# Optimization experiments

Hardware: AMD Instinct MI355X
Metric: run time of the kernel (lower is better)

## Reference

```python
import jax, jax.numpy as jnp
import numpy as np

EPS = 1e-5
NUM_HEADS = 16
HEAD_DIM = 64


def layernorm(x, g, b):
    mu = jnp.mean(x, axis=-1, keepdims=True)
    var = jnp.mean(jnp.square(x - mu), axis=-1, keepdims=True)
    return (x - mu) * jax.lax.rsqrt(var + EPS) * g + b


def setup_inputs() -> dict:
    key = jax.random.key(0)
    ks = jax.random.split(key, 10)
    B, S, Q, D = 4, 4096, 256, 1024
    x = jax.random.normal(ks[0], (B, S, D), dtype=jnp.float32)
    queries = jax.random.normal(ks[1], (B, Q, D), dtype=jnp.float32)
    attn_mask = jax.random.randint(ks[2], (B, NUM_HEADS, Q, S), 0, 2) == 1
    key_padding_mask = jax.random.randint(ks[3], (B, S), 0, 2) == 1
    scale = 1.0 / np.sqrt(2.0 * D)  # xavier-ish
    Wq = jax.random.normal(ks[4], (D, D), dtype=jnp.float32) * scale
    Wk = jax.random.normal(ks[5], (D, D), dtype=jnp.float32) * scale
    Wv = jax.random.normal(ks[6], (D, D), dtype=jnp.float32) * scale
    Wo = jax.random.normal(ks[7], (D, D), dtype=jnp.float32) * scale
    ln1_g = jnp.ones((D,), jnp.float32); ln1_b = jnp.zeros((D,), jnp.float32)
    ln2_g = jnp.ones((D,), jnp.float32); ln2_b = jnp.zeros((D,), jnp.float32)
    return {"x": x, "queries": queries, "attn_mask": attn_mask,
            "key_padding_mask": key_padding_mask, "Wq": Wq, "Wk": Wk,
            "Wv": Wv, "Wo": Wo, "ln1_g": ln1_g, "ln1_b": ln1_b,
            "ln2_g": ln2_g, "ln2_b": ln2_b}


def reference(x, queries, attn_mask, key_padding_mask, Wq, Wk, Wv, Wo,
              ln1_g, ln1_b, ln2_g, ln2_b):
    B, S, D = x.shape
    Q = queries.shape[1]
    H, hd = NUM_HEADS, HEAD_DIM

    xn = layernorm(x, ln1_g, ln1_b)
    q = (queries @ Wq.T).reshape(B, Q, H, hd)
    k = (xn @ Wk.T).reshape(B, S, H, hd)
    v = (xn @ Wv.T).reshape(B, S, H, hd)

    # scores: (B, H, Q, S)
    scores = jnp.einsum('bqhd,bshd->bhqs', q, k) / np.sqrt(hd)

    mask = attn_mask | key_padding_mask[:, None, None, :]
    neg_inf = jnp.float32(-jnp.inf)
    masked = jnp.where(mask, neg_inf, scores)
    all_masked = jnp.all(mask, axis=-1, keepdims=True)  # rows fully masked
    safe = jnp.where(all_masked, 0.0, masked)
    attn = jax.nn.softmax(safe, axis=-1)
    attn = jnp.where(all_masked, 0.0, attn)

    out = jnp.einsum('bhqs,bshd->bqhd', attn, v).reshape(B, Q, D)
    out = layernorm(out, ln2_g, ln2_b)
    return out @ Wo.T, attn.mean(axis=1)
```

## Files before the change

kernel.cpp:

```cpp
#include <hip/hip_runtime.h>
#include <math.h>

#define DEV __device__ __forceinline__

typedef float  f4v  __attribute__((ext_vector_type(4)));
typedef __bf16 b8v  __attribute__((ext_vector_type(8)));
typedef short  s8v  __attribute__((ext_vector_type(8)));

DEV short f2b(float f){ __bf16 h = (__bf16)f; return __builtin_bit_cast(short, h); }
DEV float b2f(short s){ __bf16 h = __builtin_bit_cast(__bf16, s); return (float)h; }

DEV void gload16(const void* g, void* l){
  __builtin_amdgcn_global_load_lds((const __attribute__((address_space(1))) void*)g,
                                   (__attribute__((address_space(3))) void*)l, 16, 0, 0);
}

DEV b8v ldsf(const short* p){ return __builtin_bit_cast(b8v, *(const s8v*)p); }

DEV f4v mfma16(b8v a, b8v b, f4v c){ return __builtin_amdgcn_mfma_f32_16x16x32_bf16(a, b, c, 0, 0, 0); }

DEV void lds_barrier(){
  asm volatile("s_waitcnt lgkmcnt(0)" ::: "memory");
  __builtin_amdgcn_s_barrier();
}

__global__ __launch_bounds__(256) void prep_kernel(const float* __restrict__ x, const float* __restrict__ ln1g,
                                                   const float* __restrict__ ln1b, short* __restrict__ xn,
                                                   const float* __restrict__ s0, const float* __restrict__ s1,
                                                   const float* __restrict__ s2, const float* __restrict__ s3,
                                                   const float* __restrict__ s4,
                                                   short* __restrict__ d0, short* __restrict__ d1,
                                                   short* __restrict__ d2, short* __restrict__ d3,
                                                   short* __restrict__ d4){
  int bid = blockIdx.x, tid = threadIdx.x;
  if (bid < 5120){
    int i = bid*256 + tid;
    int buf = i >> 18, j = i & 262143;
    const float* s = (buf==0)?s0:(buf==1)?s1:(buf==2)?s2:(buf==3)?s3:s4;
    short*       d = (buf==0)?d0:(buf==1)?d1:(buf==2)?d2:(buf==3)?d3:d4;
    float4 v = ((const float4*)s)[j];
    ((short4*)d)[j] = make_short4(f2b(v.x), f2b(v.y), f2b(v.z), f2b(v.w));
    return;
  }
  int row = bid - 5120;
  const float4 v = ((const float4*)(x + (size_t)row*1024))[tid];
  float s = v.x + v.y + v.z + v.w;
  #pragma unroll
  for (int off=1; off<64; off<<=1) s += __shfl_xor(s, off);
  __shared__ float red[4];
  if ((tid&63)==0) red[tid>>6] = s;
  __syncthreads();
  float mu = (red[0]+red[1]+red[2]+red[3]) * (1.0f/1024.0f);
  float e0=v.x-mu, e1=v.y-mu, e2=v.z-mu, e3=v.w-mu;
  float q = e0*e0 + e1*e1 + e2*e2 + e3*e3;
  #pragma unroll
  for (int off=1; off<64; off<<=1) q += __shfl_xor(q, off);
  __syncthreads();
  if ((tid&63)==0) red[tid>>6] = q;
  __syncthreads();
  float rs = rsqrtf((red[0]+red[1]+red[2]+red[3]) * (1.0f/1024.0f) + 1e-5f);
  float4 g4 = ((const float4*)ln1g)[tid];
  float4 b4 = ((const float4*)ln1b)[tid];
  short4 o = make_short4(f2b(e0*rs*g4.x + b4.x), f2b(e1*rs*g4.y + b4.y),
                         f2b(e2*rs*g4.z + b4.z), f2b(e3*rs*g4.w + b4.w));
  ((short4*)(xn + (size_t)row*1024))[tid] = o;
}

__global__ __launch_bounds__(256) void ln_reduce_kernel(const short* __restrict__ opart, const float* __restrict__ gg,
                                                        const float* __restrict__ bb, short* __restrict__ out){
  int row = blockIdx.x, tid = threadIdx.x;
  float a0=0.f, a1=0.f, a2=0.f, a3=0.f;
  #pragma unroll
  for (int sc=0; sc<32; ++sc){
    short4 t = ((const short4*)(opart + ((size_t)sc*1024 + row)*1024))[tid];
    a0 += b2f(t.x); a1 += b2f(t.y); a2 += b2f(t.z); a3 += b2f(t.w);
  }
  float s = a0 + a1 + a2 + a3;
  #pragma unroll
  for (int off=1; off<64; off<<=1) s += __shfl_xor(s, off);
  __shared__ float red[4];
  if ((tid&63)==0) red[tid>>6] = s;
  __syncthreads();
  float mu = (red[0]+red[1]+red[2]+red[3]) * (1.0f/1024.0f);
  float d0=a0-mu, d1=a1-mu, d2=a2-mu, d3=a3-mu;
  float q = d0*d0 + d1*d1 + d2*d2 + d3*d3;
  #pragma unroll
  for (int off=1; off<64; off<<=1) q += __shfl_xor(q, off);
  __syncthreads();
  if ((tid&63)==0) red[tid>>6] = q;
  __syncthreads();
  float rs = rsqrtf((red[0]+red[1]+red[2]+red[3]) * (1.0f/1024.0f) + 1e-5f);
  float4 g4 = ((const float4*)gg)[tid];
  float4 b4 = ((const float4*)bb)[tid];
  short4 o = make_short4(f2b(d0*rs*g4.x + b4.x), f2b(d1*rs*g4.y + b4.y),
                         f2b(d2*rs*g4.z + b4.z), f2b(d3*rs*g4.w + b4.w));
  ((short4*)(out + (size_t)row*1024))[tid] = o;
}

template<int OUTF32>
__global__ __launch_bounds__(256) void gemm_small(const short* __restrict__ A, const short* __restrict__ B,
                                                  void* __restrict__ C, int M, int N, int K){
  __shared__ short sA[2][64*64];
  __shared__ short sB[2][64*64];
  int tid=threadIdx.x, lane=tid&63, wv=tid>>6, g=lane>>4, r=lane&15;
  int wr=wv>>1, wc=wv&1;
  int m0=blockIdx.x*64, n0=blockIdx.y*64;
  f4v z = {0.f,0.f,0.f,0.f};
  f4v acc[2][2];
  #pragma unroll
  for (int i=0;i<2;++i){
    #pragma unroll
    for (int j=0;j<2;++j) acc[i][j]=z;
  }
  auto stage = [&](int buf, int kt){
    #pragma unroll
    for (int i=0;i<2;++i){
      int idx = i*256 + tid;
      int row = idx>>3, cbs = (idx&7)^(row&7);
      gload16(A + (size_t)(m0+row)*K + kt*64 + cbs*8, &sA[buf][(i*256+wv*64)*8]);
      gload16(B + (size_t)(n0+row)*K + kt*64 + cbs*8, &sB[buf][(i*256+wv*64)*8]);
    }
  };
  int nkt = K >> 6;
  stage(0, 0);
  __syncthreads();
  for (int kt=0; kt<nkt; ++kt){
    int cur = kt & 1;
    if (kt+1 < nkt) stage(cur^1, kt+1);
    b8v af[2][2], bf[2][2];
    #pragma unroll
    for (int mf=0;mf<2;++mf){
      #pragma unroll
      for (int ks=0;ks<2;++ks){
        int ra = wr*32 + mf*16 + r;
        int rb = wc*32 + mf*16 + r;
        af[mf][ks] = ldsf(&sA[cur][ra*64 + (((ks*4+g)^(ra&7))*8)]);
        bf[mf][ks] = ldsf(&sB[cur][rb*64 + (((ks*4+g)^(rb&7))*8)]);
      }
    }
    #pragma unroll
    for (int mf=0;mf<2;++mf){
      #pragma unroll
      for (int nf=0;nf<2;++nf){
        acc[mf][nf] = mfma16(af[mf][0], bf[nf][0], acc[mf][nf]);
        acc[mf][nf] = mfma16(af[mf][1], bf[nf][1], acc[mf][nf]);
      }
    }
    __syncthreads();
  }
  #pragma unroll
  for (int mf=0;mf<2;++mf){
    #pragma unroll
    for (int nf=0;nf<2;++nf){
      #pragma unroll
      for (int j=0;j<4;++j){
        int m = m0 + wr*32 + mf*16 + g*4 + j;
        int n = n0 + wc*32 + nf*16 + r;
        if (OUTF32) ((float*)C)[(size_t)m*N + n] = acc[mf][nf][j];
        else        ((short*)C)[(size_t)m*N + n] = f2b(acc[mf][nf][j]);
      }
    }
  }
}

__global__ __launch_bounds__(512,2) void gemm_dual_bt(const short* __restrict__ A, const short* __restrict__ B0,
                                                      const short* __restrict__ B1, short* __restrict__ C0,
                                                      short* __restrict__ vt, int M, int N, int K){
  __shared__ short sA[2][256*32];
  __shared__ short sB0[2][128*32];
  __shared__ short sB1[2][128*32];
  int tid=threadIdx.x, lane=tid&63, wv=tid>>6, g=lane>>4, r=lane&15;
  int wr=wv>>1, wc=wv&1;
  int m0=blockIdx.x*256, n0=blockIdx.y*128;
  f4v z = {0.f,0.f,0.f,0.f};
  f4v a0[4][4], a1[4][4];
  #pragma unroll
  for (int i=0;i<4;++i){
    #pragma unroll
    for (int j=0;j<4;++j){ a0[i][j]=z; a1[i][j]=z; }
  }
  auto stage = [&](int buf, int kt){
    #pragma unroll
    for (int i=0;i<2;++i){
      int idx = i*512 + tid;
      int row = idx>>2, sl = (idx&3)^(row&3);
      gload16(A + (size_t)(m0+row)*K + kt*32 + sl*8, &sA[buf][(i*512+wv*64)*8]);
    }
    {
      int row = tid>>2, sl = (tid&3)^(row&3);
      gload16(B0 + (size_t)(n0+row)*K + kt*32 + sl*8, &sB0[buf][(wv*64)*8]);
      gload16(B1 + (size_t)(n0+row)*K + kt*32 + sl*8, &sB1[buf][(wv*64)*8]);
    }
  };
  int nkt = K >> 5;
  stage(0, 0);
  __syncthreads();
  for (int kt=0; kt<nkt; ++kt){
    int cur = kt & 1;
    if (kt+1 < nkt) stage(cur^1, kt+1);
    b8v af[4], b0f[4], b1f[4];
    #pragma unroll
    for (int mf=0;mf<4;++mf){
      int ra = wr*64+mf*16+r;
      af[mf] = ldsf(&sA[cur][ra*32 + ((g^(ra&3))*8)]);
    }
    #pragma unroll
    for (int nf=0;nf<4;++nf){
      int rb = wc*64+nf*16+r;
      b0f[nf] = ldsf(&sB0[cur][rb*32 + ((g^(rb&3))*8)]);
      b1f[nf] = ldsf(&sB1[cur][rb*32 + ((g^(rb&3))*8)]);
    }
    #pragma unroll
    for (int mf=0;mf<4;++mf){
      #pragma unroll
      for (int nf=0;nf<4;++nf){
        a0[mf][nf] = mfma16(af[mf], b0f[nf], a0[mf][nf]);
        a1[mf][nf] = mfma16(af[mf], b1f[nf], a1[mf][nf]);
      }
    }
    __syncthreads();
  }
  int b = m0 >> 12;
  #pragma unroll
  for (int mf=0;mf<4;++mf){
    #pragma unroll
    for (int nf=0;nf<4;++nf){
      int m = m0 + wr*64 + mf*16 + g*4;
      int n = n0 + wc*64 + nf*16 + r;
      #pragma unroll
      for (int j=0;j<4;++j)
        C0[(size_t)(m+j)*N + n] = f2b(a0[mf][nf][j]);
      int h = n >> 6, hd = n & 63;
      short4 vv = make_short4(f2b(a1[mf][nf][0]), f2b(a1[mf][nf][1]),
                              f2b(a1[mf][nf][2]), f2b(a1[mf][nf][3]));
      *(short4*)&vt[(size_t)((b*16 + h)*64 + hd)*4096 + (m & 4095)] = vv;
    }
  }
}

__global__ __launch_bounds__(256,2) void lsum_kernel(const short* __restrict__ qp, const short* __restrict__ kb,
                                                     const int* __restrict__ am, const int* __restrict__ kpm,
                                                     unsigned* __restrict__ pm, float* __restrict__ lpart){
  int bid = blockIdx.x;
  int sc = bid & 15, bh = bid >> 4;
  int b = bh >> 4, h = bh & 15;
  int s0 = sc*256;
  __shared__ short sQ[256*64];
  __shared__ short sK[256*64];
  __shared__ unsigned sPM[256*8];
  int tid=threadIdx.x, lane=tid&63, wv=tid>>6, g=lane>>4, r=lane&15;

  #pragma unroll
  for (int i=0;i<8;++i){
    int idx = i*256 + wv*64 + lane;
    int row = idx>>3, cbs = (idx&7)^(row&7);
    gload16(qp + (size_t)(b*256 + row)*1024 + h*64 + cbs*8, &sQ[(i*256+wv*64)*8]);
  }
  #pragma unroll
  for (int i=0;i<8;++i){
    int idx = i*256 + wv*64 + lane;
    int row = idx>>3, cbs = (idx&7)^(row&7);
    gload16(kb + (size_t)(b*4096 + s0 + row)*1024 + h*64 + cbs*8, &sK[(i*256+wv*64)*8]);
  }
  int4 kp = *(const int4*)(kpm + (size_t)b*4096 + s0 + lane*4);
  bool k0 = kp.x!=0, k1 = kp.y!=0, k2 = kp.z!=0, k3 = kp.w!=0;
  #pragma unroll 4
  for (int i=0;i<64;++i){
    int row = wv*64 + i;
    const int4 t = *(const int4*)(am + (size_t)(bh*256 + row)*4096 + s0 + lane*4);
    unsigned long long m0 = __ballot(k0 || (t.x!=0));
    unsigned long long m1 = __ballot(k1 || (t.y!=0));
    unsigned long long m2 = __ballot(k2 || (t.z!=0));
    unsigned long long m3 = __ballot(k3 || (t.w!=0));
    if (lane < 8){
      int jj = lane>>1, hh = lane&1;
      unsigned long long bj = (jj==0)?m0:((jj==1)?m1:((jj==2)?m2:m3));
      unsigned w = (unsigned)(bj >> (hh*32));
      sPM[row*8 + lane] = w;
      pm[(size_t)bid*2048 + row*8 + lane] = w;
    }
  }
  __syncthreads();

  b8v a[4][2];
  #pragma unroll
  for (int mf=0;mf<4;++mf){
    #pragma unroll
    for (int ks=0;ks<2;++ks){
      int q = wv*64 + mf*16 + r;
      a[mf][ks] = ldsf(&sQ[q*64 + (((ks*4+g)^(q&7))*8)]);
    }
  }
  unsigned wmr[4][4][2];
  #pragma unroll
  for (int mf=0;mf<4;++mf){
    #pragma unroll
    for (int jq=0;jq<4;++jq){
      int q = wv*64 + mf*16 + g*4 + jq;
      wmr[mf][jq][0] = sPM[q*8 + (r&3)*2 + 0];
      wmr[mf][jq][1] = sPM[q*8 + (r&3)*2 + 1];
    }
  }
  float lacc[4][4];
  #pragma unroll
  for (int mf=0;mf<4;++mf){
    #pragma unroll
    for (int j=0;j<4;++j) lacc[mf][j] = 0.f;
  }
  f4v z = {0.f,0.f,0.f,0.f};
  #pragma unroll 4
  for (int nf=0;nf<16;++nf){
    int srow = nf*16 + r;
    b8v b0 = ldsf(&sK[srow*64 + ((g^(srow&7))*8)]);
    b8v b1 = ldsf(&sK[srow*64 + (((4+g)^(srow&7))*8)]);
    f4v acc[4];
    #pragma unroll
    for (int mf=0;mf<4;++mf){
      acc[mf] = mfma16(a[mf][0], b0, z);
      acc[mf] = mfma16(a[mf][1], b1, acc[mf]);
    }
    int bitp = 4*(nf&7) + (r>>2);
    #pragma unroll
    for (int mf=0;mf<4;++mf){
      #pragma unroll
      for (int j=0;j<4;++j){
        bool mskd = (wmr[mf][j][nf>>3] >> bitp) & 1u;
        lacc[mf][j] += mskd ? 0.f : __expf(acc[mf][j]*0.125f);
      }
    }
  }
  #pragma unroll
  for (int off=1; off<16; off<<=1){
    #pragma unroll
    for (int mf=0;mf<4;++mf){
      #pragma unroll
      for (int j=0;j<4;++j) lacc[mf][j] += __shfl_xor(lacc[mf][j], off);
    }
  }
  if (r == 0){
    #pragma unroll
    for (int mf=0;mf<4;++mf){
      #pragma unroll
      for (int j=0;j<4;++j){
        int q = wv*64 + mf*16 + g*4 + j;
        lpart[(size_t)bid*256 + q] = lacc[mf][j];
      }
    }
  }
}

__global__ void lcomb_kernel(const float* __restrict__ lpart, float* __restrict__ linv){
  int row = blockIdx.x*256 + threadIdx.x;
  int q = row & 255, bh = row >> 8;
  float l = 0.f;
  #pragma unroll
  for (int sc=0; sc<16; ++sc) l += lpart[(size_t)(bh*16+sc)*256 + q];
  linv[row] = (l > 0.f) ? (1.0f/l) : 0.f;
}

__global__ __launch_bounds__(512,4) void attn_pv_kernel(const short* __restrict__ qp, const short* __restrict__ kb,
                                                        const short* __restrict__ vt, const unsigned* __restrict__ pm,
                                                        const float* __restrict__ linv, short* __restrict__ opart,
                                                        float* __restrict__ out2){
  int bid = blockIdx.x;
  int sc = bid & 31, qt = (bid>>5)&3, b = bid>>7;
  int s0 = sc*128, q0 = qt*64;
  int half = sc & 1, scq = sc >> 1;
  __shared__ short sK[128*64];
  __shared__ short sV[64*128];
  __shared__ short sQ[64*64];
  __shared__ unsigned sPM[64*4];
  int tid=threadIdx.x, lane=tid&63, wv=tid>>6, g=lane>>4, r=lane&15;
  int wq = wv>>2, ws = wv&3;
  f4v z = {0.f,0.f,0.f,0.f};
  float macc[2][2][4];
  #pragma unroll
  for (int sb=0;sb<2;++sb){
    #pragma unroll
    for (int qb=0;qb<2;++qb){
      #pragma unroll
      for (int j=0;j<4;++j) macc[sb][qb][j] = 0.f;
    }
  }

  for (int h=0; h<16; ++h){
    int bh = b*16 + h;
    { int row = tid>>3, cbs = (tid&7)^(row&7);
      gload16(qp + (size_t)(b*256 + q0 + row)*1024 + h*64 + cbs*8, &sQ[(wv*64)*8]); }
    #pragma unroll
    for (int i=0;i<2;++i){
      int idx = i*512 + tid;
      int row = idx>>3, cbs = (idx&7)^(row&7);
      gload16(kb + (size_t)(b*4096 + s0 + row)*1024 + h*64 + cbs*8, &sK[(i*512+wv*64)*8]);
    }
    #pragma unroll
    for (int i=0;i<2;++i){
      int idx = i*512 + tid;
      int row = idx>>4, sl = idx&15, sls = sl^(row&7);
      gload16(vt + (size_t)(bh*64 + row)*4096 + s0 + sls*8, &sV[(i*512+wv*64)*8]);
    }
    if (tid < 256)
      sPM[tid] = pm[(size_t)(bh*16+scq)*2048 + (q0 + (tid>>2))*8 + (tid&3)*2 + half];
    __syncthreads();

    b8v qf[2][2];
    #pragma unroll
    for (int qb=0;qb<2;++qb){
      #pragma unroll
      for (int ks=0;ks<2;++ks){
        int qrow = wq*32 + qb*16 + r;
        qf[qb][ks] = ldsf(&sQ[qrow*64 + (((ks*4+g)^(qrow&7))*8)]);
      }
    }
    f4v accs[2][2];
    __builtin_amdgcn_s_setprio(1);
    #pragma unroll
    for (int sb=0;sb<2;++sb){
      int srow = ws*32 + sb*16 + r;
      b8v k0 = ldsf(&sK[srow*64 + ((g^(srow&7))*8)]);
      b8v k1 = ldsf(&sK[srow*64 + (((4+g)^(srow&7))*8)]);
      #pragma unroll
      for (int qb=0;qb<2;++qb){
        accs[sb][qb] = mfma16(k0, qf[qb][0], z);
        accs[sb][qb] = mfma16(k1, qf[qb][1], accs[sb][qb]);
      }
    }
    __builtin_amdgcn_s_setprio(0);
    lds_barrier();

    float iv[2];
    iv[0] = linv[(size_t)bh*256 + q0 + wq*32 + r];
    iv[1] = linv[(size_t)bh*256 + q0 + wq*32 + 16 + r];
    unsigned wmq[2][4];
    #pragma unroll
    for (int qb=0;qb<2;++qb){
      #pragma unroll
      for (int j=0;j<4;++j)
        wmq[qb][j] = sPM[(wq*32+qb*16+r)*4 + j];
    }
    short* P = &sK[0];
    #pragma unroll
    for (int sb=0;sb<2;++sb){
      int bitp = ws*8 + sb*4 + g;
      #pragma unroll
      for (int qb=0;qb<2;++qb){
        float pj[4];
        #pragma unroll
        for (int j=0;j<4;++j){
          bool mskd = (wmq[qb][j] >> bitp) & 1u;
          pj[j] = mskd ? 0.f : __expf(accs[sb][qb][j]*0.125f) * iv[qb];
          macc[sb][qb][j] += pj[j];
        }
        int q = wq*32 + qb*16 + r;
        unsigned lo = ((unsigned)(unsigned short)f2b(pj[0])) | (((unsigned)(unsigned short)f2b(pj[1]))<<16);
        unsigned hi = ((unsigned)(unsigned short)f2b(pj[2])) | (((unsigned)(unsigned short)f2b(pj[3]))<<16);
        int sbase = (ws*32 + sb*16 + g*4) ^ ((q&7)<<3);
        uint2 pk; pk.x = lo; pk.y = hi;
        *(uint2*)&P[q*128 + sbase] = pk;
      }
    }
    lds_barrier();

    f4v acco[2]; acco[0]=z; acco[1]=z;
    __builtin_amdgcn_s_setprio(1);
    #pragma unroll
    for (int ks=0;ks<4;++ks){
      int vrow = ws*16 + r;
      b8v bv = ldsf(&sV[vrow*128 + ((ks*32+g*8) ^ ((vrow&7)<<3))]);
      #pragma unroll
      for (int mf=0;mf<2;++mf){
        int prow = wq*32 + mf*16 + r;
        b8v ap = ldsf(&P[prow*128 + ((ks*32+g*8) ^ ((prow&7)<<3))]);
        acco[mf] = mfma16(ap, bv, acco[mf]);
      }
    }
    __builtin_amdgcn_s_setprio(0);
    #pragma unroll
    for (int mf=0;mf<2;++mf){
      #pragma unroll
      for (int j=0;j<4;++j)
        opart[((size_t)sc*1024 + b*256 + q0 + wq*32 + mf*16 + g*4 + j)*1024 + h*64 + ws*16 + r] = f2b(acco[mf][j]);
    }
    lds_barrier();
  }

  #pragma unroll
  for (int sb=0;sb<2;++sb){
    #pragma unroll
    for (int qb=0;qb<2;++qb){
      int q = q0 + wq*32 + qb*16 + r;
      float4 o = make_float4(macc[sb][qb][0]*0.0625f, macc[sb][qb][1]*0.0625f,
                             macc[sb][qb][2]*0.0625f, macc[sb][qb][3]*0.0625f);
      *(float4*)&out2[(size_t)(b*256 + q)*4096 + s0 + ws*32 + sb*16 + g*4] = o;
    }
  }
}

extern "C" void kernel_launch(void* const* d_in, const int* in_sizes, int n_in,
                              void* d_out, int out_size, void* d_ws, size_t ws_size,
                              hipStream_t stream){
  const float* x       = (const float*)d_in[0];
  const float* queries = (const float*)d_in[1];
  const int*   am      = (const int*)d_in[2];
  const int*   kpm     = (const int*)d_in[3];
  const float* Wq      = (const float*)d_in[4];
  const float* Wk      = (const float*)d_in[5];
  const float* Wv      = (const float*)d_in[6];
  const float* Wo      = (const float*)d_in[7];
  const float* ln1g    = (const float*)d_in[8];
  const float* ln1b    = (const float*)d_in[9];
  const float* ln2g    = (const float*)d_in[10];
  const float* ln2b    = (const float*)d_in[11];
  float* out0 = (float*)d_out;
  float* out2 = out0 + (size_t)4*256*1024;
  char* ws = (char*)d_ws;

  size_t off = 0;
  auto alloc = [&](size_t bytes){ void* p = ws + off; off += (bytes + 255) & ~(size_t)255; return p; };
  short*    xn   = (short*)alloc(33554432);
  short*    kb   = (short*)alloc(33554432);
  short*    vt   = (short*)alloc(33554432);
  short*    wqb  = (short*)alloc(2097152);
  short*    wkb  = (short*)alloc(2097152);
  short*    wvb  = (short*)alloc(2097152);
  short*    wob  = (short*)alloc(2097152);
  short*    qbf  = (short*)alloc(2097152);
  short*    qpj  = (short*)alloc(2097152);
  unsigned* pmw  = (unsigned*)alloc(8388608);
  float*    lpart= (float*)alloc(1048576);
  float*    linv = (float*)alloc(65536);
  short*    opart= (short*)alloc(67108864);
  short*    onb  = (short*)alloc(2097152);

  prep_kernel<<<21504,256,0,stream>>>(x, ln1g, ln1b, xn,
                                      queries, Wq, Wk, Wv, Wo, qbf, wqb, wkb, wvb, wob);
  gemm_dual_bt<<<dim3(64,8),512,0,stream>>>(xn, wkb, wvb, kb, vt, 16384, 1024, 1024);
  gemm_small<0><<<dim3(16,16),256,0,stream>>>(qbf, wqb, qpj, 1024, 1024, 1024);
  lsum_kernel<<<1024,256,0,stream>>>(qpj, kb, am, kpm, pmw, lpart);
  lcomb_kernel<<<64,256,0,stream>>>(lpart, linv);
  attn_pv_kernel<<<512,512,0,stream>>>(qpj, kb, vt, pmw, linv, opart, out2);
  ln_reduce_kernel<<<1024,256,0,stream>>>(opart, ln2g, ln2b, onb);
  gemm_small<1><<<dim3(16,16),256,0,stream>>>(onb, wob, out0, 1024, 1024, 1024);
}
```

Before: 323.1 us.

## Split attention into head-mean kernel and per-head PV kernel accumulating over S

The fused attention/PV kernel is split into two kernels. One computes only the head-averaged attention probabilities, looping over heads per S-chunk. The other loops over S-chunks per (batch, head, q-tile) and keeps the PV accumulator in registers, so only 2 partial outputs are written instead of 32. This greatly reduces the opart write/read traffic and shrinks the LN reduce, but it recomputes QK^T and exp in both kernels. Q fragments are also now loaded straight from global memory instead of through LDS.

Result: slower. 346.2 us (+7.2%).

```diff
diff --git a/kernel.cpp b/kernel.cpp
--- a/kernel.cpp
+++ b/kernel.cpp
@@ -16,6 +16,7 @@
 }
 
 DEV b8v ldsf(const short* p){ return __builtin_bit_cast(b8v, *(const s8v*)p); }
+DEV b8v gldf(const short* p){ return __builtin_bit_cast(b8v, *(const s8v*)p); }
 
 DEV f4v mfma16(b8v a, b8v b, f4v c){ return __builtin_amdgcn_mfma_f32_16x16x32_bf16(a, b, c, 0, 0, 0); }
 
@@ -66,12 +67,12 @@
   ((short4*)(xn + (size_t)row*1024))[tid] = o;
 }
 
-__global__ __launch_bounds__(256) void ln_reduce_kernel(const short* __restrict__ opart, const float* __restrict__ gg,
-                                                        const float* __restrict__ bb, short* __restrict__ out){
+__global__ __launch_bounds__(256) void ln_reduce2_kernel(const short* __restrict__ opart, const float* __restrict__ gg,
+                                                         const float* __restrict__ bb, short* __restrict__ out){
   int row = blockIdx.x, tid = threadIdx.x;
   float a0=0.f, a1=0.f, a2=0.f, a3=0.f;
   #pragma unroll
-  for (int sc=0; sc<32; ++sc){
+  for (int sc=0; sc<2; ++sc){
     short4 t = ((const short4*)(opart + ((size_t)sc*1024 + row)*1024))[tid];
     a0 += b2f(t.x); a1 += b2f(t.y); a2 += b2f(t.z); a3 += b2f(t.w);
   }
@@ -358,17 +359,15 @@
   linv[row] = (l > 0.f) ? (1.0f/l) : 0.f;
 }
 
-__global__ __launch_bounds__(512,4) void attn_pv_kernel(const short* __restrict__ qp, const short* __restrict__ kb,
-                                                        const short* __restrict__ vt, const unsigned* __restrict__ pm,
-                                                        const float* __restrict__ linv, short* __restrict__ opart,
-                                                        float* __restrict__ out2){
+__global__ __launch_bounds__(512,4) void attn_out2_kernel(const short* __restrict__ qp, const short* __restrict__ kb,
+                                                          const unsigned* __restrict__ pm,
+                                                          const float* __restrict__ linv,
+                                                          float* __restrict__ out2){
   int bid = blockIdx.x;
   int sc = bid & 31, qt = (bid>>5)&3, b = bid>>7;
   int s0 = sc*128, q0 = qt*64;
   int half = sc & 1, scq = sc >> 1;
   __shared__ short sK[128*64];
-  __shared__ short sV[64*128];
-  __shared__ short sQ[64*64];
   __shared__ unsigned sPM[64*4];
   int tid=threadIdx.x, lane=tid&63, wv=tid>>6, g=lane>>4, r=lane&15;
   int wq = wv>>2, ws = wv&3;
@@ -385,33 +384,24 @@
 
   for (int h=0; h<16; ++h){
     int bh = b*16 + h;
-    { int row = tid>>3, cbs = (tid&7)^(row&7);
-      gload16(qp + (size_t)(b*256 + q0 + row)*1024 + h*64 + cbs*8, &sQ[(wv*64)*8]); }
+    __syncthreads();
     #pragma unroll
     for (int i=0;i<2;++i){
       int idx = i*512 + tid;
       int row = idx>>3, cbs = (idx&7)^(row&7);
       gload16(kb + (size_t)(b*4096 + s0 + row)*1024 + h*64 + cbs*8, &sK[(i*512+wv*64)*8]);
     }
-    #pragma unroll
-    for (int i=0;i<2;++i){
-      int idx = i*512 + tid;
-      int row = idx>>4, sl = idx&15, sls = sl^(row&7);
-      gload16(vt + (size_t)(bh*64 + row)*4096 + s0 + sls*8, &sV[(i*512+wv*64)*8]);
-    }
     if (tid < 256)
       sPM[tid] = pm[(size_t)(bh*16+scq)*2048 + (q0 + (tid>>2))*8 + (tid&3)*2 + half];
+    b8v qf[2][2];
+    #pragma unroll
+    for (int qb=0;qb<2;++qb){
+      #pragma unroll
+      for (int ks=0;ks<2;++ks)
+        qf[qb][ks] = gldf(qp + (size_t)(b*256 + q0 + wq*32 + qb*16 + r)*1024 + h*64 + (ks*4+g)*8);
+    }
     __syncthreads();
 
-    b8v qf[2][2];
-    #pragma unroll
-    for (int qb=0;qb<2;++qb){
-      #pragma unroll
-      for (int ks=0;ks<2;++ks){
-        int qrow = wq*32 + qb*16 + r;
-        qf[qb][ks] = ldsf(&sQ[qrow*64 + (((ks*4+g)^(qrow&7))*8)]);
-      }
-    }
     f4v accs[2][2];
     __builtin_amdgcn_s_setprio(1);
     #pragma unroll
@@ -426,11 +416,106 @@
       }
     }
     __builtin_amdgcn_s_setprio(0);
-    lds_barrier();
 
     float iv[2];
     iv[0] = linv[(size_t)bh*256 + q0 + wq*32 + r];
     iv[1] = linv[(size_t)bh*256 + q0 + wq*32 + 16 + r];
+    unsigned wmq[2][4];
+    #pragma unroll
+    for (int qb=0;qb<2;++qb){
+      #pragma unroll
+      for (int j=0;j<4;++j)
+        wmq[qb][j] = sPM[(wq*32+qb*16+r)*4 + j];
+    }
+    #pragma unroll
+    for (int sb=0;sb<2;++sb){
+      int bitp = ws*8 + sb*4 + g;
+      #pragma unroll
+      for (int qb=0;qb<2;++qb){
+        #pragma unroll
+        for (int j=0;j<4;++j){
+          bool mskd = (wmq[qb][j] >> bitp) & 1u;
+          macc[sb][qb][j] += mskd ? 0.f : __expf(accs[sb][qb][j]*0.125f) * iv[qb];
+        }
+      }
+    }
+  }
+
+  #pragma unroll
+  for (int sb=0;sb<2;++sb){
+    #pragma unroll
+    for (int qb=0;qb<2;++qb){
+      int q = q0 + wq*32 + qb*16 + r;
+      float4 o = make_float4(macc[sb][qb][0]*0.0625f, macc[sb][qb][1]*0.0625f,
+                             macc[sb][qb][2]*0.0625f, macc[sb][qb][3]*0.0625f);
+      *(float4*)&out2[(size_t)(b*256 + q)*4096 + s0 + ws*32 + sb*16 + g*4] = o;
+    }
+  }
+}
+
+__global__ __launch_bounds__(512,4) void attn_o_kernel(const short* __restrict__ qp, const short* __restrict__ kb,
+                                                       const short* __restrict__ vt, const unsigned* __restrict__ pm,
+                                                       const float* __restrict__ linv, short* __restrict__ opart){
+  int bid = blockIdx.x;
+  int sch = bid & 1, qt = (bid>>1)&3, h = (bid>>3)&15, b = bid>>7;
+  int q0 = qt*64, bh = b*16 + h;
+  __shared__ short sK[128*64];
+  __shared__ short sV[64*128];
+  __shared__ unsigned sPM[64*4];
+  int tid=threadIdx.x, lane=tid&63, wv=tid>>6, g=lane>>4, r=lane&15;
+  int wq = wv>>2, ws = wv&3;
+  f4v z = {0.f,0.f,0.f,0.f};
+
+  b8v qf[2][2];
+  #pragma unroll
+  for (int qb=0;qb<2;++qb){
+    #pragma unroll
+    for (int ks=0;ks<2;++ks)
+      qf[qb][ks] = gldf(qp + (size_t)(b*256 + q0 + wq*32 + qb*16 + r)*1024 + h*64 + (ks*4+g)*8);
+  }
+  float iv[2];
+  iv[0] = linv[(size_t)bh*256 + q0 + wq*32 + r];
+  iv[1] = linv[(size_t)bh*256 + q0 + wq*32 + 16 + r];
+
+  f4v acco[2]; acco[0]=z; acco[1]=z;
+
+  for (int i=0; i<16; ++i){
+    int sc = sch*16 + i;
+    int s0 = sc*128;
+    int half = sc & 1, scq = sc >> 1;
+    __syncthreads();
+    #pragma unroll
+    for (int ii=0;ii<2;++ii){
+      int idx = ii*512 + tid;
+      int row = idx>>3, cbs = (idx&7)^(row&7);
+      gload16(kb + (size_t)(b*4096 + s0 + row)*1024 + h*64 + cbs*8, &sK[(ii*512+wv*64)*8]);
+    }
+    #pragma unroll
+    for (int ii=0;ii<2;++ii){
+      int idx = ii*512 + tid;
+      int row = idx>>4, sl = idx&15, sls = sl^(row&7);
+      gload16(vt + (size_t)(bh*64 + row)*4096 + s0 + sls*8, &sV[(ii*512+wv*64)*8]);
+    }
+    if (tid < 256)
+      sPM[tid] = pm[(size_t)(bh*16+scq)*2048 + (q0 + (tid>>2))*8 + (tid&3)*2 + half];
+    __syncthreads();
+
+    f4v accs[2][2];
+    __builtin_amdgcn_s_setprio(1);
+    #pragma unroll
+    for (int sb=0;sb<2;++sb){
+      int srow = ws*32 + sb*16 + r;
+      b8v k0 = ldsf(&sK[srow*64 + ((g^(srow&7))*8)]);
+      b8v k1 = ldsf(&sK[srow*64 + (((4+g)^(srow&7))*8)]);
+      #pragma unroll
+      for (int qb=0;qb<2;++qb){
+        accs[sb][qb] = mfma16(k0, qf[qb][0], z);
+        accs[sb][qb] = mfma16(k1, qf[qb][1], accs[sb][qb]);
+      }
+    }
+    __builtin_amdgcn_s_setprio(0);
+    lds_barrier();
+
     unsigned wmq[2][4];
     #pragma unroll
     for (int qb=0;qb<2;++qb){
@@ -449,7 +534,6 @@
         for (int j=0;j<4;++j){
           bool mskd = (wmq[qb][j] >> bitp) & 1u;
           pj[j] = mskd ? 0.f : __expf(accs[sb][qb][j]*0.125f) * iv[qb];
-          macc[sb][qb][j] += pj[j];
         }
         int q = wq*32 + qb*16 + r;
         unsigned lo = ((unsigned)(unsigned short)f2b(pj[0])) | (((unsigned)(unsigned short)f2b(pj[1]))<<16);
@@ -461,7 +545,6 @@
     }
     lds_barrier();
 
-    f4v acco[2]; acco[0]=z; acco[1]=z;
     __builtin_amdgcn_s_setprio(1);
     #pragma unroll
     for (int ks=0;ks<4;++ks){
@@ -475,24 +558,13 @@
       }
     }
     __builtin_amdgcn_s_setprio(0);
-    #pragma unroll
-    for (int mf=0;mf<2;++mf){
-      #pragma unroll
-      for (int j=0;j<4;++j)
-        opart[((size_t)sc*1024 + b*256 + q0 + wq*32 + mf*16 + g*4 + j)*1024 + h*64 + ws*16 + r] = f2b(acco[mf][j]);
-    }
-    lds_barrier();
-  }
-
-  #pragma unroll
-  for (int sb=0;sb<2;++sb){
-    #pragma unroll
-    for (int qb=0;qb<2;++qb){
-      int q = q0 + wq*32 + qb*16 + r;
-      float4 o = make_float4(macc[sb][qb][0]*0.0625f, macc[sb][qb][1]*0.0625f,
-                             macc[sb][qb][2]*0.0625f, macc[sb][qb][3]*0.0625f);
-      *(float4*)&out2[(size_t)(b*256 + q)*4096 + s0 + ws*32 + sb*16 + g*4] = o;
-    }
+  }
+
+  #pragma unroll
+  for (int mf=0;mf<2;++mf){
+    #pragma unroll
+    for (int j=0;j<4;++j)
+      opart[((size_t)sch*1024 + b*256 + q0 + wq*32 + mf*16 + g*4 + j)*1024 + h*64 + ws*16 + r] = f2b(acco[mf][j]);
   }
 }
 
@@ -529,7 +601,7 @@
   unsigned* pmw  = (unsigned*)alloc(8388608);
   float*    lpart= (float*)alloc(1048576);
   float*    linv = (float*)alloc(65536);
-  short*    opart= (short*)alloc(67108864);
+  short*    opart= (short*)alloc(4194304);
   short*    onb  = (short*)alloc(2097152);
 
   prep_kernel<<<21504,256,0,stream>>>(x, ln1g, ln1b, xn,
@@ -538,7 +610,8 @@
   gemm_small<0><<<dim3(16,16),256,0,stream>>>(qbf, wqb, qpj, 1024, 1024, 1024);
   lsum_kernel<<<1024,256,0,stream>>>(qpj, kb, am, kpm, pmw, lpart);
   lcomb_kernel<<<64,256,0,stream>>>(lpart, linv);
-  attn_pv_kernel<<<512,512,0,stream>>>(qpj, kb, vt, pmw, linv, opart, out2);
-  ln_reduce_kernel<<<1024,256,0,stream>>>(opart, ln2g, ln2b, onb);
+  attn_out2_kernel<<<512,512,0,stream>>>(qpj, kb, pmw, linv, out2);
+  attn_o_kernel<<<512,512,0,stream>>>(qpj, kb, vt, pmw, linv, opart);
+  ln_reduce2_kernel<<<1024,256,0,stream>>>(opart, ln2g, ln2b, onb);
   gemm_small<1><<<dim3(16,16),256,0,stream>>>(onb, wob, out0, 1024, 1024, 1024);
 }
```

## Use partial vmcnt waits in GEMM pipelines and load Q fragments directly from global

Applied to the files above, without the earlier changes.

Both GEMM loops replace the full __syncthreads with an explicit s_waitcnt vmcnt(4) plus barrier, so the current tile can be consumed while the next tile's global-to-LDS loads are still in flight. This aims to expose real double-buffer overlap instead of draining all memory ops each iteration. In the attention PV kernel, the Q tile is no longer staged through LDS; each wave loads its Q fragments straight from global memory into registers, removing an LDS buffer and one staging round trip. This adds redundant global reads of Q across waves, and the vmcnt counts must match the number of outstanding loads per thread exactly.

New measurement: 346.5 us. +7.3%, slower.

```diff
diff --git a/kernel.cpp b/kernel.cpp
--- a/kernel.cpp
+++ b/kernel.cpp
@@ -16,6 +16,7 @@
 }
 
 DEV b8v ldsf(const short* p){ return __builtin_bit_cast(b8v, *(const s8v*)p); }
+DEV b8v gldf(const short* p){ return __builtin_bit_cast(b8v, *(const s8v*)p); }
 
 DEV f4v mfma16(b8v a, b8v b, f4v c){ return __builtin_amdgcn_mfma_f32_16x16x32_bf16(a, b, c, 0, 0, 0); }
 
@@ -123,10 +124,15 @@
   };
   int nkt = K >> 6;
   stage(0, 0);
-  __syncthreads();
   for (int kt=0; kt<nkt; ++kt){
     int cur = kt & 1;
-    if (kt+1 < nkt) stage(cur^1, kt+1);
+    if (kt+1 < nkt){
+      stage(cur^1, kt+1);
+      asm volatile("s_waitcnt vmcnt(4)" ::: "memory");
+    } else {
+      asm volatile("s_waitcnt vmcnt(0)" ::: "memory");
+    }
+    __builtin_amdgcn_s_barrier();
     b8v af[2][2], bf[2][2];
     #pragma unroll
     for (int mf=0;mf<2;++mf){
@@ -146,7 +152,8 @@
         acc[mf][nf] = mfma16(af[mf][1], bf[nf][1], acc[mf][nf]);
       }
     }
-    __syncthreads();
+    asm volatile("s_waitcnt lgkmcnt(0)" ::: "memory");
+    __builtin_amdgcn_s_barrier();
   }
   #pragma unroll
   for (int mf=0;mf<2;++mf){
@@ -194,10 +201,15 @@
   };
   int nkt = K >> 5;
   stage(0, 0);
-  __syncthreads();
   for (int kt=0; kt<nkt; ++kt){
     int cur = kt & 1;
-    if (kt+1 < nkt) stage(cur^1, kt+1);
+    if (kt+1 < nkt){
+      stage(cur^1, kt+1);
+      asm volatile("s_waitcnt vmcnt(4)" ::: "memory");
+    } else {
+      asm volatile("s_waitcnt vmcnt(0)" ::: "memory");
+    }
+    __builtin_amdgcn_s_barrier();
     b8v af[4], b0f[4], b1f[4];
     #pragma unroll
     for (int mf=0;mf<4;++mf){
@@ -218,7 +230,8 @@
         a1[mf][nf] = mfma16(af[mf], b1f[nf], a1[mf][nf]);
       }
     }
-    __syncthreads();
+    asm volatile("s_waitcnt lgkmcnt(0)" ::: "memory");
+    __builtin_amdgcn_s_barrier();
   }
   int b = m0 >> 12;
   #pragma unroll
@@ -368,7 +381,6 @@
   int half = sc & 1, scq = sc >> 1;
   __shared__ short sK[128*64];
   __shared__ short sV[64*128];
-  __shared__ short sQ[64*64];
   __shared__ unsigned sPM[64*4];
   int tid=threadIdx.x, lane=tid&63, wv=tid>>6, g=lane>>4, r=lane&15;
   int wq = wv>>2, ws = wv&3;
@@ -385,8 +397,6 @@
 
   for (int h=0; h<16; ++h){
     int bh = b*16 + h;
-    { int row = tid>>3, cbs = (tid&7)^(row&7);
-      gload16(qp + (size_t)(b*256 + q0 + row)*1024 + h*64 + cbs*8, &sQ[(wv*64)*8]); }
     #pragma unroll
     for (int i=0;i<2;++i){
       int idx = i*512 + tid;
@@ -401,17 +411,15 @@
     }
     if (tid < 256)
       sPM[tid] = pm[(size_t)(bh*16+scq)*2048 + (q0 + (tid>>2))*8 + (tid&3)*2 + half];
+    b8v qf[2][2];
+    #pragma unroll
+    for (int qb=0;qb<2;++qb){
+      #pragma unroll
+      for (int ks=0;ks<2;++ks)
+        qf[qb][ks] = gldf(qp + (size_t)(b*256 + q0 + wq*32 + qb*16 + r)*1024 + h*64 + (ks*4+g)*8);
+    }
     __syncthreads();
 
-    b8v qf[2][2];
-    #pragma unroll
-    for (int qb=0;qb<2;++qb){
-      #pragma unroll
-      for (int ks=0;ks<2;++ks){
-        int qrow = wq*32 + qb*16 + r;
-        qf[qb][ks] = ldsf(&sQ[qrow*64 + (((ks*4+g)^(qrow&7))*8)]);
-      }
-    }
     f4v accs[2][2];
     __builtin_amdgcn_s_setprio(1);
     #pragma unroll
```
